# Kernel tuning notes

Measured on AMD Instinct MI355X. Metric: run time of the kernel, lower is better.

The kernel has to match this reference:

```python
import jax, jax.numpy as jnp
import numpy as np

EMBED_DIM = 32
PIC_RES = 96
KERNEL_BW = 3.0
STEP_SIZE = 0.5
NB_ITERS = 3


def setup_inputs() -> dict:
    key = jax.random.key(0)
    # scale down so exp(bw * x^T x) stays in a safe numeric range
    x_in = jax.random.normal(key, (1, EMBED_DIM, PIC_RES, PIC_RES), dtype=jnp.float32) * 0.1
    return {"x_in": x_in}


def reference(x_in):
    # x: [D, N], N = res*res pixels
    x = x_in.reshape(EMBED_DIM, -1)
    outs = []
    for _ in range(NB_ITERS):
        # affinity K[i,j] = exp(bw * <x_i, x_j>), shape [N, N]
        K = jnp.exp(KERNEL_BW * (x.T @ x))
        # column sums d_j = sum_i K[i,j] (== torch diag(K^T @ 1)); K is symmetric
        d = K.sum(axis=0)
        # x <- x @ (step * K diag(1/d) + (1-step) I)
        x = STEP_SIZE * (x @ K) / d + (1.0 - STEP_SIZE) * x
        outs.append(x.reshape(EMBED_DIM, PIC_RES, PIC_RES))
    final = x.reshape(EMBED_DIM, PIC_RES, PIC_RES)
    return final, jnp.stack(outs)
```

## Files before the change

kernel.cpp:

```cpp
#include <hip/hip_runtime.h>
#include <hip/hip_bf16.h>
#include <math.h>


#define D 32
#define NPIX 9216
#define NSPLIT 16
#define JB 128
#define NJB (NPIX / JB)
#define IPB (NPIX / NSPLIT)
#define XST 56
#define WST 56
#define TS  40

typedef __attribute__((ext_vector_type(8))) short short8;
typedef __attribute__((ext_vector_type(4))) float f32x4;
typedef __attribute__((ext_vector_type(2))) unsigned int u32x2;

#if __has_builtin(__builtin_amdgcn_exp2f)
#define EXP2F __builtin_amdgcn_exp2f
#else
#define EXP2F exp2f
#endif

#define C3 4.32808512266689f

__device__ __forceinline__ unsigned pack2_bf16(float a, float b) {
    union { __hip_bfloat162 h2; unsigned u; } c;
    c.h2 = __float22bfloat162_rn(make_float2(a, b));
    return c.u;
}
__device__ __forceinline__ short pack1_bf16(float a) {
    union { __hip_bfloat16 h; unsigned short s; } c;
    c.h = __float2bfloat16(a);
    return (short)c.s;
}

__global__ __launch_bounds__(256) void accum_kernel(
    const short* __restrict__ xb,
    const short* __restrict__ xbT,
    float* __restrict__ num, float* __restrict__ den)
{
    __shared__ __align__(16) short xiT_s[32 * XST];
    __shared__ __align__(16) short xi_s [32 * XST];
    __shared__ __align__(16) short w_s[4][2][16 * WST];

    const int t = threadIdx.x;
    const int wid = t >> 6, lane = t & 63, quad = lane >> 4, m = lane & 15;
    const int bj = blockIdx.x % NJB, bi = blockIdx.x / NJB;
    const int j0 = bj * JB + wid * 32;
    const int i0b = bi * IPB;

    short8 bfrag[2];
#pragma unroll
    for (int jt = 0; jt < 2; ++jt)
        bfrag[jt] = *(const short8*)&xbT[(j0 + jt * 16 + m) * D + quad * 8];

    f32x4 acc[2][2] = {};
    float dacc[2] = {0.f, 0.f};

    const int s_r = t >> 3, s_c = (t & 7) * 4;

    for (int ic = 0; ic < IPB; ic += 32) {
        const int i0 = i0b + ic;
        __syncthreads();
        *(u32x2*)&xiT_s[s_r * XST + s_c] = *(const u32x2*)&xbT[(i0 + s_r) * D + s_c];
        *(u32x2*)&xi_s [s_r * XST + s_c] = *(const u32x2*)&xb [s_r * NPIX + i0 + s_c];
        __syncthreads();

        short8 aT[2], aV[2];
#pragma unroll
        for (int it = 0; it < 2; ++it)
            aT[it] = *(const short8*)&xiT_s[(it * 16 + m) * XST + quad * 8];
#pragma unroll
        for (int dt = 0; dt < 2; ++dt)
            aV[dt] = *(const short8*)&xi_s[(dt * 16 + m) * XST + quad * 8];

#pragma unroll
        for (int jt = 0; jt < 2; ++jt) {
            f32x4 z = {0.f, 0.f, 0.f, 0.f};
            f32x4 s0 = __builtin_amdgcn_mfma_f32_16x16x32_bf16(aT[0], bfrag[jt], z, 0, 0, 0);
            f32x4 s1 = __builtin_amdgcn_mfma_f32_16x16x32_bf16(aT[1], bfrag[jt], z, 0, 0, 0);

            float w[8];
#pragma unroll
            for (int r = 0; r < 4; ++r) { w[r]     = EXP2F(C3 * s0[r]);
                                          w[4 + r] = EXP2F(C3 * s1[r]); }
#pragma unroll
            for (int r = 0; r < 8; ++r) dacc[jt] += w[r];

            u32x2 p0, p1;
            p0.x = pack2_bf16(w[0], w[1]); p0.y = pack2_bf16(w[2], w[3]);
            p1.x = pack2_bf16(w[4], w[5]); p1.y = pack2_bf16(w[6], w[7]);
            *(u32x2*)&w_s[wid][jt][m * WST +      quad * 4] = p0;
            *(u32x2*)&w_s[wid][jt][m * WST + 16 + quad * 4] = p1;

            short8 wb = *(const short8*)&w_s[wid][jt][m * WST + quad * 8];

            acc[0][jt] = __builtin_amdgcn_mfma_f32_16x16x32_bf16(aV[0], wb, acc[0][jt], 0, 0, 0);
            acc[1][jt] = __builtin_amdgcn_mfma_f32_16x16x32_bf16(aV[1], wb, acc[1][jt], 0, 0, 0);
        }
    }

#pragma unroll
    for (int dt = 0; dt < 2; ++dt)
#pragma unroll
        for (int jt = 0; jt < 2; ++jt)
#pragma unroll
            for (int r = 0; r < 4; ++r)
                atomicAdd(&num[(dt * 16 + quad * 4 + r) * NPIX + j0 + jt * 16 + m],
                          acc[dt][jt][r]);
#pragma unroll
    for (int jt = 0; jt < 2; ++jt) {
        float v = dacc[jt];
        v += __shfl_xor(v, 16, 64);
        v += __shfl_xor(v, 32, 64);
        if (quad == 0) atomicAdd(&den[j0 + jt * 16 + m], v);
    }
}

__global__ __launch_bounds__(256) void combine_kernel(
    const float* __restrict__ xin, float* __restrict__ num,
    float* __restrict__ den, float* __restrict__ xout,
    float* __restrict__ xfinal, short* __restrict__ xb, short* __restrict__ xbT,
    int do_ms)
{
    __shared__ __align__(16) short tile[64 * TS];
    const int t = threadIdx.x;
    const int il = t & 63, q = t >> 6;
    const int i = blockIdx.x * 64 + il;
    const int d0 = q * 8;

    float inv = 0.f;
    if (do_ms) inv = 0.5f / den[i];

#pragma unroll
    for (int dd = 0; dd < 8; ++dd) {
        const int d = d0 + dd;
        const int idx = d * NPIX + i;
        float v;
        if (do_ms) {
            v = num[idx] * inv + 0.5f * xin[idx];
            xout[idx] = v;
            if (xfinal) xfinal[idx] = v;
        } else {
            v = xin[idx];
        }
        num[idx] = 0.f;
        short b = pack1_bf16(v);
        xb[idx] = b;
        tile[il * TS + d] = b;
    }
    __syncthreads();
    if (q == 0) den[i] = 0.f;
    *(short8*)&xbT[i * D + d0] = *(const short8*)&tile[il * TS + d0];
}

extern "C" void kernel_launch(void* const* d_in, const int* in_sizes, int n_in,
                              void* d_out, int out_size, void* d_ws, size_t ws_size,
                              hipStream_t stream)
{
    const float* x0 = (const float*)d_in[0];
    float* out = (float*)d_out;
    const size_t slot = (size_t)D * NPIX;

    float* num = (float*)d_ws;
    float* den = num + slot;
    short* xb  = (short*)(den + NPIX);
    short* xbT = xb + slot;

    combine_kernel<<<dim3(NPIX / 64), dim3(256), 0, stream>>>(
        x0, num, den, nullptr, nullptr, xb, xbT, 0);

    for (int t = 0; t < 3; ++t) {
        accum_kernel<<<dim3(NJB * NSPLIT), dim3(256), 0, stream>>>(xb, xbT, num, den);
        const float* xin = (t == 0) ? x0 : (out + (size_t)t * slot);
        combine_kernel<<<dim3(NPIX / 64), dim3(256), 0, stream>>>(
            xin, num, den, out + (size_t)(t + 1) * slot,
            (t == 2) ? out : nullptr, xb, xbT, 1);
    }
}
```

Before: 178.6 us.

## Replace atomic accumulation with per-split partial buffers and double i-chunk per barrier

The accumulate kernel no longer atomically adds into shared num/den arrays. Each i-split now writes its own partial buffer, and the combine kernel sums the 16 partials, which also removes the need to zero num/den. The inner loop also loads 64 i-rows per barrier pair using 16-byte loads into double-sized shared tiles, halving the number of syncs. The cost is 16x more workspace and extra global reads in combine, which must now read 16 partial slices per output.

Result: slower. 188.9 us (+5.8%).

```diff
diff --git a/kernel.cpp b/kernel.cpp
--- a/kernel.cpp
+++ b/kernel.cpp
@@ -9,6 +9,7 @@
 #define JB 128
 #define NJB (NPIX / JB)
 #define IPB (NPIX / NSPLIT)
+#define ICH 64
 #define XST 56
 #define WST 56
 #define TS  40
@@ -39,10 +40,11 @@
 __global__ __launch_bounds__(256) void accum_kernel(
     const short* __restrict__ xb,
     const short* __restrict__ xbT,
-    float* __restrict__ num, float* __restrict__ den)
+    float* __restrict__ num_part,
+    float* __restrict__ den_part)
 {
-    __shared__ __align__(16) short xiT_s[32 * XST];
-    __shared__ __align__(16) short xi_s [32 * XST];
+    __shared__ __align__(16) short xiT_s[2][32 * XST];
+    __shared__ __align__(16) short xi_s [2][32 * XST];
     __shared__ __align__(16) short w_s[4][2][16 * WST];
 
     const int t = threadIdx.x;
@@ -59,71 +61,77 @@
     f32x4 acc[2][2] = {};
     float dacc[2] = {0.f, 0.f};
 
-    const int s_r = t >> 3, s_c = (t & 7) * 4;
+    const int srT = t >> 2,  scT = (t & 3) * 8;
+    const int srV = t >> 3,  cV = (t & 7) >> 2, qV = ((t & 3)) * 8;
 
-    for (int ic = 0; ic < IPB; ic += 32) {
+    for (int ic = 0; ic < IPB; ic += ICH) {
         const int i0 = i0b + ic;
         __syncthreads();
-        *(u32x2*)&xiT_s[s_r * XST + s_c] = *(const u32x2*)&xbT[(i0 + s_r) * D + s_c];
-        *(u32x2*)&xi_s [s_r * XST + s_c] = *(const u32x2*)&xb [s_r * NPIX + i0 + s_c];
+        *(short8*)&xiT_s[srT >> 5][(srT & 31) * XST + scT] =
+            *(const short8*)&xbT[(i0 + srT) * D + scT];
+        *(short8*)&xi_s[cV][srV * XST + qV] =
+            *(const short8*)&xb[srV * NPIX + i0 + cV * 32 + qV];
         __syncthreads();
 
-        short8 aT[2], aV[2];
 #pragma unroll
-        for (int it = 0; it < 2; ++it)
-            aT[it] = *(const short8*)&xiT_s[(it * 16 + m) * XST + quad * 8];
+        for (int h = 0; h < 2; ++h) {
+            short8 aT[2], aV[2];
 #pragma unroll
-        for (int dt = 0; dt < 2; ++dt)
-            aV[dt] = *(const short8*)&xi_s[(dt * 16 + m) * XST + quad * 8];
+            for (int it = 0; it < 2; ++it)
+                aT[it] = *(const short8*)&xiT_s[h][(it * 16 + m) * XST + quad * 8];
+#pragma unroll
+            for (int dt = 0; dt < 2; ++dt)
+                aV[dt] = *(const short8*)&xi_s[h][(dt * 16 + m) * XST + quad * 8];
 
 #pragma unroll
-        for (int jt = 0; jt < 2; ++jt) {
-            f32x4 z = {0.f, 0.f, 0.f, 0.f};
-            f32x4 s0 = __builtin_amdgcn_mfma_f32_16x16x32_bf16(aT[0], bfrag[jt], z, 0, 0, 0);
-            f32x4 s1 = __builtin_amdgcn_mfma_f32_16x16x32_bf16(aT[1], bfrag[jt], z, 0, 0, 0);
+            for (int jt = 0; jt < 2; ++jt) {
+                f32x4 z = {0.f, 0.f, 0.f, 0.f};
+                f32x4 s0 = __builtin_amdgcn_mfma_f32_16x16x32_bf16(aT[0], bfrag[jt], z, 0, 0, 0);
+                f32x4 s1 = __builtin_amdgcn_mfma_f32_16x16x32_bf16(aT[1], bfrag[jt], z, 0, 0, 0);
 
-            float w[8];
+                float w[8];
 #pragma unroll
-            for (int r = 0; r < 4; ++r) { w[r]     = EXP2F(C3 * s0[r]);
-                                          w[4 + r] = EXP2F(C3 * s1[r]); }
+                for (int r = 0; r < 4; ++r) { w[r]     = EXP2F(C3 * s0[r]);
+                                              w[4 + r] = EXP2F(C3 * s1[r]); }
 #pragma unroll
-            for (int r = 0; r < 8; ++r) dacc[jt] += w[r];
+                for (int r = 0; r < 8; ++r) dacc[jt] += w[r];
 
-            u32x2 p0, p1;
-            p0.x = pack2_bf16(w[0], w[1]); p0.y = pack2_bf16(w[2], w[3]);
-            p1.x = pack2_bf16(w[4], w[5]); p1.y = pack2_bf16(w[6], w[7]);
-            *(u32x2*)&w_s[wid][jt][m * WST +      quad * 4] = p0;
-            *(u32x2*)&w_s[wid][jt][m * WST + 16 + quad * 4] = p1;
+                u32x2 p0, p1;
+                p0.x = pack2_bf16(w[0], w[1]); p0.y = pack2_bf16(w[2], w[3]);
+                p1.x = pack2_bf16(w[4], w[5]); p1.y = pack2_bf16(w[6], w[7]);
+                *(u32x2*)&w_s[wid][jt][m * WST +      quad * 4] = p0;
+                *(u32x2*)&w_s[wid][jt][m * WST + 16 + quad * 4] = p1;
 
-            short8 wb = *(const short8*)&w_s[wid][jt][m * WST + quad * 8];
+                short8 wb = *(const short8*)&w_s[wid][jt][m * WST + quad * 8];
 
-            acc[0][jt] = __builtin_amdgcn_mfma_f32_16x16x32_bf16(aV[0], wb, acc[0][jt], 0, 0, 0);
-            acc[1][jt] = __builtin_amdgcn_mfma_f32_16x16x32_bf16(aV[1], wb, acc[1][jt], 0, 0, 0);
+                acc[0][jt] = __builtin_amdgcn_mfma_f32_16x16x32_bf16(aV[0], wb, acc[0][jt], 0, 0, 0);
+                acc[1][jt] = __builtin_amdgcn_mfma_f32_16x16x32_bf16(aV[1], wb, acc[1][jt], 0, 0, 0);
+            }
         }
     }
 
+    float* np = num_part + (size_t)bi * D * NPIX;
 #pragma unroll
     for (int dt = 0; dt < 2; ++dt)
 #pragma unroll
         for (int jt = 0; jt < 2; ++jt)
 #pragma unroll
             for (int r = 0; r < 4; ++r)
-                atomicAdd(&num[(dt * 16 + quad * 4 + r) * NPIX + j0 + jt * 16 + m],
-                          acc[dt][jt][r]);
+                np[(dt * 16 + quad * 4 + r) * NPIX + j0 + jt * 16 + m] = acc[dt][jt][r];
 #pragma unroll
     for (int jt = 0; jt < 2; ++jt) {
         float v = dacc[jt];
         v += __shfl_xor(v, 16, 64);
         v += __shfl_xor(v, 32, 64);
-        if (quad == 0) atomicAdd(&den[j0 + jt * 16 + m], v);
+        if (quad == 0) den_part[bi * NPIX + j0 + jt * 16 + m] = v;
     }
 }
 
 __global__ __launch_bounds__(256) void combine_kernel(
-    const float* __restrict__ xin, float* __restrict__ num,
-    float* __restrict__ den, float* __restrict__ xout,
-    float* __restrict__ xfinal, short* __restrict__ xb, short* __restrict__ xbT,
-    int do_ms)
+    const float* __restrict__ xin,
+    const float* __restrict__ num_part, const float* __restrict__ den_part,
+    float* __restrict__ xout, float* __restrict__ xfinal,
+    short* __restrict__ xb, short* __restrict__ xbT, int do_ms)
 {
     __shared__ __align__(16) short tile[64 * TS];
     const int t = threadIdx.x;
@@ -132,7 +140,12 @@
     const int d0 = q * 8;
 
     float inv = 0.f;
-    if (do_ms) inv = 0.5f / den[i];
+    if (do_ms) {
+        float den = 0.f;
+#pragma unroll
+        for (int s = 0; s < NSPLIT; ++s) den += den_part[s * NPIX + i];
+        inv = 0.5f / den;
+    }
 
 #pragma unroll
     for (int dd = 0; dd < 8; ++dd) {
@@ -140,19 +153,20 @@
         const int idx = d * NPIX + i;
         float v;
         if (do_ms) {
-            v = num[idx] * inv + 0.5f * xin[idx];
+            float nm = 0.f;
+#pragma unroll
+            for (int s = 0; s < NSPLIT; ++s) nm += num_part[(s * D + d) * NPIX + i];
+            v = nm * inv + 0.5f * xin[idx];
             xout[idx] = v;
             if (xfinal) xfinal[idx] = v;
         } else {
             v = xin[idx];
         }
-        num[idx] = 0.f;
         short b = pack1_bf16(v);
         xb[idx] = b;
         tile[il * TS + d] = b;
     }
     __syncthreads();
-    if (q == 0) den[i] = 0.f;
     *(short8*)&xbT[i * D + d0] = *(const short8*)&tile[il * TS + d0];
 }
 
@@ -164,19 +178,20 @@
     float* out = (float*)d_out;
     const size_t slot = (size_t)D * NPIX;
 
-    float* num = (float*)d_ws;
-    float* den = num + slot;
-    short* xb  = (short*)(den + NPIX);
+    float* num_part = (float*)d_ws;
+    float* den_part = num_part + (size_t)NSPLIT * slot;
+    short* xb  = (short*)(den_part + (size_t)NSPLIT * NPIX);
     short* xbT = xb + slot;
 
     combine_kernel<<<dim3(NPIX / 64), dim3(256), 0, stream>>>(
-        x0, num, den, nullptr, nullptr, xb, xbT, 0);
+        x0, nullptr, nullptr, nullptr, nullptr, xb, xbT, 0);
 
     for (int t = 0; t < 3; ++t) {
-        accum_kernel<<<dim3(NJB * NSPLIT), dim3(256), 0, stream>>>(xb, xbT, num, den);
+        accum_kernel<<<dim3(NJB * NSPLIT), dim3(256), 0, stream>>>(
+            xb, xbT, num_part, den_part);
         const float* xin = (t == 0) ? x0 : (out + (size_t)t * slot);
         combine_kernel<<<dim3(NPIX / 64), dim3(256), 0, stream>>>(
-            xin, num, den, out + (size_t)(t + 1) * slot,
+            xin, num_part, den_part, out + (size_t)(t + 1) * slot,
             (t == 2) ? out : nullptr, xb, xbT, 1);
     }
 }
```
